# Performance work log

Hardware: AMD Instinct MI355X
Metric: run time of the kernel (lower is better)

Reference implementation:

```python
import jax, jax.numpy as jnp
import numpy as np

N_NODES = 100000
N_EDGES = 1600000
D_FEAT = 48


def setup_inputs() -> dict:
    key = jax.random.key(0)
    k1, k2, k3, k4 = jax.random.split(key, 4)
    rows = jax.random.randint(k1, (N_EDGES,), 0, N_NODES, dtype=jnp.int32)
    cols = jax.random.randint(k2, (N_EDGES,), 0, N_NODES, dtype=jnp.int32)
    vals = jax.random.uniform(k3, (N_EDGES,), dtype=jnp.float32)
    embeds = jax.random.normal(k4, (N_NODES, D_FEAT), dtype=jnp.float32)
    return {"rows": rows, "cols": cols, "vals": vals, "embeds": embeds}


def reference(rows, cols, vals, embeds):
    # out = spmm(adj, embeds): out[r] = sum_{e: rows[e]==r} vals[e] * embeds[cols[e]]
    msgs = vals[:, None] * embeds[cols]  # [E, d] gather + scale
    out = jax.ops.segment_sum(msgs, rows, num_segments=embeds.shape[0])  # [N, d]
    return out
```

## Files before the change

### kernel.cpp

```cpp
#include <hip/hip_runtime.h>
#include <hip/hip_fp16.h>


#define N_NODES 100000
#define N_EDGES 1600000
#define D_FEAT  48

#define R_PER_BUCKET 128
#define NBUCKETS ((N_NODES + R_PER_BUCKET - 1) / R_PER_BUCKET)
#define NWG 256
#define CHUNK ((N_EDGES + NWG - 1) / NWG)
#define MAT (NBUCKETS * NWG)
#define SCAN_CHUNK 1024
#define NB_SCAN ((MAT + SCAN_CHUNK - 1) / SCAN_CHUNK)
#define CONV_N4 ((N_NODES * D_FEAT) / 4)
#define CONV_BLK ((CONV_N4 + 511) / 512)
#define CAP 3072

__global__ __launch_bounds__(512) void count_convert(const int* __restrict__ rows,
                                                     unsigned int* __restrict__ mat,
                                                     const float4* __restrict__ esrc,
                                                     __half2* __restrict__ edst) {
    const int t = threadIdx.x;
    if (blockIdx.x < NWG) {
        __shared__ unsigned int lc[NBUCKETS];
        const int w = blockIdx.x;
        for (int i = t; i < NBUCKETS; i += 512) lc[i] = 0u;
        __syncthreads();
        const int lo = w * CHUNK;
        const int hi = (lo + CHUNK < N_EDGES) ? lo + CHUNK : N_EDGES;
        for (int e = lo + t; e < hi; e += 512)
            atomicAdd(&lc[rows[e] >> 7], 1u);
        __syncthreads();
        for (int b = t; b < NBUCKETS; b += 512)
            mat[b * NWG + w] = lc[b];
    } else {
        int i = (blockIdx.x - NWG) * 512 + t;
        if (i < CONV_N4) {
            float4 v = esrc[i];
            edst[2 * i]     = __floats2half2_rn(v.x, v.y);
            edst[2 * i + 1] = __floats2half2_rn(v.z, v.w);
        }
    }
}

__global__ __launch_bounds__(256) void scan_phase1(const unsigned int* __restrict__ mat,
                                                   unsigned int* __restrict__ bsum) {
    __shared__ unsigned int s[256];
    const int blk = blockIdx.x, t = threadIdx.x;
    const int base = blk * SCAN_CHUNK + t * 4;
    unsigned int sum = 0;
#pragma unroll
    for (int k = 0; k < 4; ++k) {
        int i = base + k;
        if (i < MAT) sum += mat[i];
    }
    s[t] = sum;
    __syncthreads();
    for (int off = 128; off > 0; off >>= 1) {
        if (t < off) s[t] += s[t + off];
        __syncthreads();
    }
    if (t == 0) bsum[blk] = s[0];
}

__global__ __launch_bounds__(256) void scan_phase3(unsigned int* __restrict__ mat,
                                                   const unsigned int* __restrict__ bsum,
                                                   unsigned int* __restrict__ bstart) {
    __shared__ unsigned int s[256];
    __shared__ unsigned int bpre[256];
    const int blk = blockIdx.x, t = threadIdx.x;
    bpre[t] = (t < NB_SCAN) ? bsum[t] : 0u;
    __syncthreads();
    for (int off = 1; off < 256; off <<= 1) {
        unsigned int u = (t >= off) ? bpre[t - off] : 0u;
        __syncthreads();
        bpre[t] += u;
        __syncthreads();
    }
    const unsigned int blkbase = (blk == 0) ? 0u : bpre[blk - 1];

    const int base = blk * SCAN_CHUNK + t * 4;
    unsigned int c[4];
    unsigned int sum = 0;
#pragma unroll
    for (int k = 0; k < 4; ++k) {
        int i = base + k;
        c[k] = (i < MAT) ? mat[i] : 0u;
        sum += c[k];
    }
    s[t] = sum;
    __syncthreads();
    for (int off = 1; off < 256; off <<= 1) {
        unsigned int u = (t >= off) ? s[t - off] : 0u;
        __syncthreads();
        s[t] += u;
        __syncthreads();
    }
    unsigned int prefix = blkbase + ((t == 0) ? 0u : s[t - 1]);
#pragma unroll
    for (int k = 0; k < 4; ++k) {
        int i = base + k;
        if (i < MAT) {
            mat[i] = prefix;
            if ((i & (NWG - 1)) == 0) bstart[i / NWG] = prefix;
            prefix += c[k];
        }
    }
    if (blk == 0 && t == 0) bstart[NBUCKETS] = N_EDGES;
}

__global__ __launch_bounds__(512) void place_kernel(const int* __restrict__ rows,
                                                    const int* __restrict__ cols,
                                                    const float* __restrict__ vals,
                                                    const unsigned int* __restrict__ mat,
                                                    int2* __restrict__ buf1) {
    __shared__ unsigned int lc[NBUCKETS];
    const int w = blockIdx.x, t = threadIdx.x;
    for (int b = t; b < NBUCKETS; b += 512) lc[b] = mat[b * NWG + w];
    __syncthreads();
    const int lo = w * CHUNK;
    const int hi = (lo + CHUNK < N_EDGES) ? lo + CHUNK : N_EDGES;
    for (int e = lo + t; e < hi; e += 512) {
        int r = rows[e];
        unsigned int pos = atomicAdd(&lc[r >> 7], 1u);
        buf1[pos] = make_int2(((r & 127) << 17) | cols[e], __float_as_int(vals[e]));
    }
}

__global__ __launch_bounds__(512) void finalize_spmm(const unsigned int* __restrict__ bstart,
                                                     const int2* __restrict__ buf1,
                                                     const __half2* __restrict__ embeds_h2,
                                                     float* __restrict__ out) {
    __shared__ unsigned int sedge[CAP];
    __shared__ unsigned int rstart[R_PER_BUCKET + 1];
    __shared__ unsigned int rc[R_PER_BUCKET];
    __shared__ unsigned int sscan[R_PER_BUCKET];
    const int b = blockIdx.x, t = threadIdx.x;
    const unsigned int S = bstart[b];
    const unsigned int E = bstart[b + 1];
    const unsigned int cnt = E - S;
    const int g   = t >> 5;
    const int sub = t & 31;
    const bool act = sub < 24;
    const int row0 = b * R_PER_BUCKET;

#define PROC(q)                                                       \
    {                                                                 \
        union { __half h; unsigned short u; } hv;                     \
        hv.u = (unsigned short)((q) >> 17);                           \
        float vv = __half2float(hv.h);                                \
        __half2 e2 = embeds_h2[((q) & 0x1FFFFu) * 24 + sub];          \
        ax = fmaf(vv, __low2float(e2), ax);                           \
        ay = fmaf(vv, __high2float(e2), ay);                          \
    }

    if (cnt <= CAP) {
        if (t < R_PER_BUCKET) rc[t] = 0u;
        __syncthreads();
        for (unsigned int j = S + t; j < E; j += 512)
            atomicAdd(&rc[(unsigned)buf1[j].x >> 17], 1u);
        __syncthreads();
        if (t < R_PER_BUCKET) sscan[t] = rc[t];
        __syncthreads();
        for (int off = 1; off < R_PER_BUCKET; off <<= 1) {
            unsigned int u = 0;
            if (t < R_PER_BUCKET && t >= off) u = sscan[t - off];
            __syncthreads();
            if (t < R_PER_BUCKET && t >= off) sscan[t] += u;
            __syncthreads();
        }
        if (t < R_PER_BUCKET) {
            unsigned int pre = (t == 0) ? 0u : sscan[t - 1];
            rstart[t] = pre;
            rc[t] = pre;
        }
        if (t == 0) rstart[R_PER_BUCKET] = cnt;
        __syncthreads();
        for (unsigned int j = S + t; j < E; j += 512) {
            int2 cv = buf1[j];
            unsigned int pos = atomicAdd(&rc[(unsigned)cv.x >> 17], 1u);
            union { __half h; unsigned short u; } hv;
            hv.h = __float2half_rn(__int_as_float(cv.y));
            sedge[pos] = ((unsigned int)hv.u << 17) | ((unsigned)cv.x & 0x1FFFFu);
        }
        __syncthreads();

        for (int rr = g * 8; rr < g * 8 + 8; ++rr) {
            int row = row0 + rr;
            if (row >= N_NODES) break;
            unsigned int j = rstart[rr], end = rstart[rr + 1];
            float ax = 0.f, ay = 0.f;
            for (; j + 8 <= end; j += 8) {
                unsigned int q0 = sedge[j + 0];
                unsigned int q1 = sedge[j + 1];
                unsigned int q2 = sedge[j + 2];
                unsigned int q3 = sedge[j + 3];
                unsigned int q4 = sedge[j + 4];
                unsigned int q5 = sedge[j + 5];
                unsigned int q6 = sedge[j + 6];
                unsigned int q7 = sedge[j + 7];
                if (act) {
                    PROC(q0) PROC(q1) PROC(q2) PROC(q3)
                    PROC(q4) PROC(q5) PROC(q6) PROC(q7)
                }
            }
            for (; j < end; ++j) {
                unsigned int q = sedge[j];
                if (act) PROC(q)
            }
            if (act)
                *(float2*)(out + (size_t)row * D_FEAT + sub * 2) = make_float2(ax, ay);
        }
    } else {
        for (int rr = g * 8; rr < g * 8 + 8; ++rr) {
            int row = row0 + rr;
            if (row >= N_NODES) break;
            float ax = 0.f, ay = 0.f;
            for (unsigned int j = S; j < E; ++j) {
                int2 cv = buf1[j];
                if (((unsigned)cv.x >> 17) == (unsigned)rr && act) {
                    union { __half h; unsigned short u; } hv;
                    hv.h = __float2half_rn(__int_as_float(cv.y));
                    unsigned int q = ((unsigned int)hv.u << 17) | ((unsigned)cv.x & 0x1FFFFu);
                    PROC(q)
                }
            }
            if (act)
                *(float2*)(out + (size_t)row * D_FEAT + sub * 2) = make_float2(ax, ay);
        }
    }
#undef PROC
}

__global__ __launch_bounds__(256) void zero_out_kernel(float4* __restrict__ out, int n4) {
    int i = blockIdx.x * 256 + threadIdx.x;
    if (i < n4) out[i] = make_float4(0.f, 0.f, 0.f, 0.f);
}
__global__ __launch_bounds__(256) void spmm_atomic_kernel(const int* __restrict__ rows,
                                                          const int* __restrict__ cols,
                                                          const float* __restrict__ vals,
                                                          const float* __restrict__ embeds,
                                                          float* __restrict__ out) {
    long long tid = (long long)blockIdx.x * 256 + threadIdx.x;
    const long long total = (long long)N_EDGES * 12;
    if (tid >= total) return;
    int e = (int)(tid / 12), q = (int)(tid % 12);
    int r = rows[e], c = cols[e];
    float v = vals[e];
    const float4 emb = *(const float4*)(embeds + (long long)c * D_FEAT + q * 4);
    float* o = out + (long long)r * D_FEAT + q * 4;
    atomicAdd(o + 0, v * emb.x);
    atomicAdd(o + 1, v * emb.y);
    atomicAdd(o + 2, v * emb.z);
    atomicAdd(o + 3, v * emb.w);
}

extern "C" void kernel_launch(void* const* d_in, const int* in_sizes, int n_in,
                              void* d_out, int out_size, void* d_ws, size_t ws_size,
                              hipStream_t stream) {
    const int*   rows   = (const int*)d_in[0];
    const int*   cols   = (const int*)d_in[1];
    const float* vals   = (const float*)d_in[2];
    const float* embeds = (const float*)d_in[3];
    float*       out    = (float*)d_out;

    unsigned int* mat = (unsigned int*)d_ws;
    size_t mat_bytes  = ((size_t)MAT * 4 + 15) & ~(size_t)15;
    unsigned int* bstart = (unsigned int*)((char*)d_ws + mat_bytes);
    size_t bs_bytes   = (((size_t)(NBUCKETS + 1) * 4) + 15) & ~(size_t)15;
    unsigned int* bsum = (unsigned int*)((char*)d_ws + mat_bytes + bs_bytes);
    size_t bsum_bytes = (((size_t)NB_SCAN * 4) + 15) & ~(size_t)15;
    int2* buf1 = (int2*)((char*)d_ws + mat_bytes + bs_bytes + bsum_bytes);
    __half2* embeds_h2 = (__half2*)((char*)buf1 + (size_t)N_EDGES * 8);
    size_t need = mat_bytes + bs_bytes + bsum_bytes +
                  (size_t)N_EDGES * 8 + (size_t)N_NODES * D_FEAT * 2;

    if (ws_size < need) {
        int n4 = out_size / 4;
        zero_out_kernel<<<(n4 + 255) / 256, 256, 0, stream>>>((float4*)out, n4);
        long long total = (long long)N_EDGES * 12;
        spmm_atomic_kernel<<<(int)((total + 255) / 256), 256, 0, stream>>>(rows, cols, vals, embeds, out);
        return;
    }

    count_convert<<<NWG + CONV_BLK, 512, 0, stream>>>(rows, mat,
                                                      (const float4*)embeds, embeds_h2);
    scan_phase1<<<NB_SCAN, 256, 0, stream>>>(mat, bsum);
    scan_phase3<<<NB_SCAN, 256, 0, stream>>>(mat, bsum, bstart);
    place_kernel<<<NWG, 512, 0, stream>>>(rows, cols, vals, mat, buf1);
    finalize_spmm<<<NBUCKETS, 512, 0, stream>>>(bstart, buf1, embeds_h2, out);
}
```

Baseline: 81.50 us.

## Quantize embeddings to per-row int8 and shrink row buckets to 96

Embeddings are quantized to int8 with a per-row fp16 scale, stored in 64-byte rows, replacing the fp16 copy. This halves gather bytes per edge and aligns each gathered row to a 64-byte line. Buckets shrink from 128 to 96 rows, using a multiply-high divide, with matching CAP, per-group row counts and scan chunk size. The change adds quantization error beyond fp16, so accuracy tolerance is at risk.

Measured after the change: 101.2 us. +24.2%, slower.

```diff
diff --git a/kernel.cpp b/kernel.cpp
--- a/kernel.cpp
+++ b/kernel.cpp
@@ -6,21 +6,24 @@
 #define N_EDGES 1600000
 #define D_FEAT  48
 
-#define R_PER_BUCKET 128
-#define NBUCKETS ((N_NODES + R_PER_BUCKET - 1) / R_PER_BUCKET)
+#define RPB 96
+#define NBUCKETS ((N_NODES + RPB - 1) / RPB)
 #define NWG 256
 #define CHUNK ((N_EDGES + NWG - 1) / NWG)
 #define MAT (NBUCKETS * NWG)
-#define SCAN_CHUNK 1024
+#define SCAN_CHUNK 2048
 #define NB_SCAN ((MAT + SCAN_CHUNK - 1) / SCAN_CHUNK)
-#define CONV_N4 ((N_NODES * D_FEAT) / 4)
-#define CONV_BLK ((CONV_N4 + 511) / 512)
-#define CAP 3072
+#define CONV_WGS (N_NODES / 8)
+#define CAP 2048
+
+__device__ __forceinline__ unsigned bucket_of(unsigned r) {
+    return __umulhi(r, 2863311531u) >> 6;
+}
 
 __global__ __launch_bounds__(512) void count_convert(const int* __restrict__ rows,
                                                      unsigned int* __restrict__ mat,
-                                                     const float4* __restrict__ esrc,
-                                                     __half2* __restrict__ edst) {
+                                                     const float2* __restrict__ esrc,
+                                                     unsigned short* __restrict__ embq) {
     const int t = threadIdx.x;
     if (blockIdx.x < NWG) {
         __shared__ unsigned int lc[NBUCKETS];
@@ -30,17 +33,28 @@
         const int lo = w * CHUNK;
         const int hi = (lo + CHUNK < N_EDGES) ? lo + CHUNK : N_EDGES;
         for (int e = lo + t; e < hi; e += 512)
-            atomicAdd(&lc[rows[e] >> 7], 1u);
+            atomicAdd(&lc[bucket_of((unsigned)rows[e])], 1u);
         __syncthreads();
         for (int b = t; b < NBUCKETS; b += 512)
             mat[b * NWG + w] = lc[b];
     } else {
-        int i = (blockIdx.x - NWG) * 512 + t;
-        if (i < CONV_N4) {
-            float4 v = esrc[i];
-            edst[2 * i]     = __floats2half2_rn(v.x, v.y);
-            edst[2 * i + 1] = __floats2half2_rn(v.z, v.w);
-        }
+        const int row  = (blockIdx.x - NWG) * 8 + (t >> 6);
+        const int lane = t & 63;
+        float2 v = make_float2(0.f, 0.f);
+        if (lane < 24) v = esrc[(size_t)row * 24 + lane];
+        float m = fmaxf(fabsf(v.x), fabsf(v.y));
+#pragma unroll
+        for (int mask = 1; mask <= 32; mask <<= 1)
+            m = fmaxf(m, __shfl_xor(m, mask));
+        float inv = (m > 0.f) ? 127.f / m : 0.f;
+        if (lane < 24) {
+            int lo = __float2int_rn(v.x * inv);
+            int hi = __float2int_rn(v.y * inv);
+            unsigned short p = (unsigned short)((lo & 0xff) | ((hi & 0xff) << 8));
+            embq[(size_t)row * 32 + lane] = p;
+        }
+        if (lane == 24)
+            embq[(size_t)row * 32 + 24] = __half_as_ushort(__float2half(m * (1.f / 127.f)));
     }
 }
 
@@ -48,10 +62,10 @@
                                                    unsigned int* __restrict__ bsum) {
     __shared__ unsigned int s[256];
     const int blk = blockIdx.x, t = threadIdx.x;
-    const int base = blk * SCAN_CHUNK + t * 4;
+    const int base = blk * SCAN_CHUNK + t * 8;
     unsigned int sum = 0;
 #pragma unroll
-    for (int k = 0; k < 4; ++k) {
+    for (int k = 0; k < 8; ++k) {
         int i = base + k;
         if (i < MAT) sum += mat[i];
     }
@@ -80,11 +94,11 @@
     }
     const unsigned int blkbase = (blk == 0) ? 0u : bpre[blk - 1];
 
-    const int base = blk * SCAN_CHUNK + t * 4;
-    unsigned int c[4];
+    const int base = blk * SCAN_CHUNK + t * 8;
+    unsigned int c[8];
     unsigned int sum = 0;
 #pragma unroll
-    for (int k = 0; k < 4; ++k) {
+    for (int k = 0; k < 8; ++k) {
         int i = base + k;
         c[k] = (i < MAT) ? mat[i] : 0u;
         sum += c[k];
@@ -99,11 +113,11 @@
     }
     unsigned int prefix = blkbase + ((t == 0) ? 0u : s[t - 1]);
 #pragma unroll
-    for (int k = 0; k < 4; ++k) {
+    for (int k = 0; k < 8; ++k) {
         int i = base + k;
         if (i < MAT) {
             mat[i] = prefix;
-            if ((i & (NWG - 1)) == 0) bstart[i / NWG] = prefix;
+            if ((i & (NWG - 1)) == 0) bstart[i >> 8] = prefix;
             prefix += c[k];
         }
     }
@@ -122,20 +136,23 @@
     const int lo = w * CHUNK;
     const int hi = (lo + CHUNK < N_EDGES) ? lo + CHUNK : N_EDGES;
     for (int e = lo + t; e < hi; e += 512) {
-        int r = rows[e];
-        unsigned int pos = atomicAdd(&lc[r >> 7], 1u);
-        buf1[pos] = make_int2(((r & 127) << 17) | cols[e], __float_as_int(vals[e]));
+        unsigned r = (unsigned)rows[e];
+        unsigned b = bucket_of(r);
+        unsigned lr = r - b * RPB;
+        unsigned int pos = atomicAdd(&lc[b], 1u);
+        buf1[pos] = make_int2((int)((lr << 17) | (unsigned)cols[e]),
+                              __float_as_int(vals[e]));
     }
 }
 
 __global__ __launch_bounds__(512) void finalize_spmm(const unsigned int* __restrict__ bstart,
                                                      const int2* __restrict__ buf1,
-                                                     const __half2* __restrict__ embeds_h2,
+                                                     const unsigned short* __restrict__ embq,
                                                      float* __restrict__ out) {
     __shared__ unsigned int sedge[CAP];
-    __shared__ unsigned int rstart[R_PER_BUCKET + 1];
-    __shared__ unsigned int rc[R_PER_BUCKET];
-    __shared__ unsigned int sscan[R_PER_BUCKET];
+    __shared__ unsigned int rstart[RPB + 1];
+    __shared__ unsigned int rc[RPB];
+    __shared__ unsigned int sscan[RPB];
     const int b = blockIdx.x, t = threadIdx.x;
     const unsigned int S = bstart[b];
     const unsigned int E = bstart[b + 1];
@@ -143,39 +160,42 @@
     const int g   = t >> 5;
     const int sub = t & 31;
     const bool act = sub < 24;
-    const int row0 = b * R_PER_BUCKET;
-
-#define PROC(q)                                                       \
-    {                                                                 \
-        union { __half h; unsigned short u; } hv;                     \
-        hv.u = (unsigned short)((q) >> 17);                           \
-        float vv = __half2float(hv.h);                                \
-        __half2 e2 = embeds_h2[((q) & 0x1FFFFu) * 24 + sub];          \
-        ax = fmaf(vv, __low2float(e2), ax);                           \
-        ay = fmaf(vv, __high2float(e2), ay);                          \
+    const int row0 = b * RPB;
+
+#define PROC(q)                                                          \
+    {                                                                    \
+        unsigned col = (q) & 0x1FFFFu;                                   \
+        const unsigned short* rp = embq + ((size_t)col << 5);            \
+        unsigned short qq = rp[sub];                                     \
+        float sc = __half2float(__ushort_as_half(rp[24]));               \
+        float vs = __half2float(__ushort_as_half((unsigned short)((q) >> 17))) * sc; \
+        float lo = (float)(int)(signed char)(qq & 0xff);                 \
+        float hi = (float)(int)(signed char)(qq >> 8);                   \
+        ax = fmaf(vs, lo, ax);                                           \
+        ay = fmaf(vs, hi, ay);                                           \
     }
 
     if (cnt <= CAP) {
-        if (t < R_PER_BUCKET) rc[t] = 0u;
+        if (t < RPB) rc[t] = 0u;
         __syncthreads();
         for (unsigned int j = S + t; j < E; j += 512)
             atomicAdd(&rc[(unsigned)buf1[j].x >> 17], 1u);
         __syncthreads();
-        if (t < R_PER_BUCKET) sscan[t] = rc[t];
-        __syncthreads();
-        for (int off = 1; off < R_PER_BUCKET; off <<= 1) {
+        if (t < RPB) sscan[t] = rc[t];
+        __syncthreads();
+        for (int off = 1; off < RPB; off <<= 1) {
             unsigned int u = 0;
-            if (t < R_PER_BUCKET && t >= off) u = sscan[t - off];
+            if (t < RPB && t >= off) u = sscan[t - off];
             __syncthreads();
-            if (t < R_PER_BUCKET && t >= off) sscan[t] += u;
+            if (t < RPB && t >= off) sscan[t] += u;
             __syncthreads();
         }
-        if (t < R_PER_BUCKET) {
+        if (t < RPB) {
             unsigned int pre = (t == 0) ? 0u : sscan[t - 1];
             rstart[t] = pre;
             rc[t] = pre;
         }
-        if (t == 0) rstart[R_PER_BUCKET] = cnt;
+        if (t == 0) rstart[RPB] = cnt;
         __syncthreads();
         for (unsigned int j = S + t; j < E; j += 512) {
             int2 cv = buf1[j];
@@ -186,7 +206,7 @@
         }
         __syncthreads();
 
-        for (int rr = g * 8; rr < g * 8 + 8; ++rr) {
+        for (int rr = g * 6; rr < g * 6 + 6; ++rr) {
             int row = row0 + rr;
             if (row >= N_NODES) break;
             unsigned int j = rstart[rr], end = rstart[rr + 1];
@@ -213,7 +233,7 @@
                 *(float2*)(out + (size_t)row * D_FEAT + sub * 2) = make_float2(ax, ay);
         }
     } else {
-        for (int rr = g * 8; rr < g * 8 + 8; ++rr) {
+        for (int rr = g * 6; rr < g * 6 + 6; ++rr) {
             int row = row0 + rr;
             if (row >= N_NODES) break;
             float ax = 0.f, ay = 0.f;
@@ -272,9 +292,9 @@
     unsigned int* bsum = (unsigned int*)((char*)d_ws + mat_bytes + bs_bytes);
     size_t bsum_bytes = (((size_t)NB_SCAN * 4) + 15) & ~(size_t)15;
     int2* buf1 = (int2*)((char*)d_ws + mat_bytes + bs_bytes + bsum_bytes);
-    __half2* embeds_h2 = (__half2*)((char*)buf1 + (size_t)N_EDGES * 8);
+    unsigned short* embq = (unsigned short*)((char*)buf1 + (size_t)N_EDGES * 8);
     size_t need = mat_bytes + bs_bytes + bsum_bytes +
-                  (size_t)N_EDGES * 8 + (size_t)N_NODES * D_FEAT * 2;
+                  (size_t)N_EDGES * 8 + (size_t)N_NODES * 64;
 
     if (ws_size < need) {
         int n4 = out_size / 4;
@@ -284,10 +304,10 @@
         return;
     }
 
-    count_convert<<<NWG + CONV_BLK, 512, 0, stream>>>(rows, mat,
-                                                      (const float4*)embeds, embeds_h2);
+    count_convert<<<NWG + CONV_WGS, 512, 0, stream>>>(rows, mat,
+                                                      (const float2*)embeds, embq);
     scan_phase1<<<NB_SCAN, 256, 0, stream>>>(mat, bsum);
     scan_phase3<<<NB_SCAN, 256, 0, stream>>>(mat, bsum, bstart);
     place_kernel<<<NWG, 512, 0, stream>>>(rows, cols, vals, mat, buf1);
-    finalize_spmm<<<NBUCKETS, 512, 0, stream>>>(bstart, buf1, embeds_h2, out);
-}
+    finalize_spmm<<<NBUCKETS, 512, 0, stream>>>(bstart, buf1, embq, out);
+}
```
